# Kernel tuning notes

Hardware: AMD Instinct MI355X
Metric: run time of the kernel (lower is better)

The kernel has to match this reference:

```python
import jax, jax.numpy as jnp
import numpy as np

N_NODES = 30000
N_EDGES = 480000
N_REL = 16
DIM = 128
N_TRIPLES = 200000


def _xavier(key, shape):
    fan_in, fan_out = shape[-2], shape[-1]
    limit = np.sqrt(6.0 / (fan_in + fan_out)).astype(np.float32)
    return jax.random.uniform(key, shape, jnp.float32, -limit, limit)


def setup_inputs() -> dict:
    key = jax.random.key(0)
    ks = jax.random.split(key, 12)
    inp = {
        "node_emb": _xavier(ks[0], (N_NODES, DIM)),
        "rel_emb": _xavier(ks[1], (N_REL, DIM)),
        "W_rel0": _xavier(ks[2], (N_REL, DIM, DIM)),
        "Wself_w0": _xavier(ks[3], (DIM, DIM)),
        "Wself_b0": jnp.zeros((DIM,), jnp.float32),
        "W_rel1": _xavier(ks[4], (N_REL, DIM, DIM)),
        "Wself_w1": _xavier(ks[5], (DIM, DIM)),
        "Wself_b1": jnp.zeros((DIM,), jnp.float32),
        "local_nodes": jnp.arange(N_NODES, dtype=jnp.int32),
        "edge_index": jax.random.randint(ks[6], (2, N_EDGES), 0, N_NODES, jnp.int32),
        "edge_type": jax.random.randint(ks[7], (N_EDGES,), 0, N_REL, jnp.int32),
        "h_loc": jax.random.randint(ks[8], (N_TRIPLES,), 0, N_NODES, jnp.int32),
        "r_ids": jax.random.randint(ks[9], (N_TRIPLES,), 0, N_REL, jnp.int32),
        "t_loc": jax.random.randint(ks[10], (N_TRIPLES,), 0, N_NODES, jnp.int32),
    }
    return inp


def _rgcn_layer(x, edge_index, edge_type, W_rel, Ww, Wb):
    # x: [N, in], W_rel: [R, in, out], Ww: [out, in] (torch Linear layout)
    N = x.shape[0]
    out = x @ Ww.T + Wb                                 # self loop [N, out]
    src, dst = edge_index[0], edge_index[1]
    # transform every node under every relation, then gather per edge:
    # math-equivalent to bmm(x[src][:,None,:], W_rel[rel]) in the original,
    # but avoids materializing [E, in, out].
    xt = jnp.einsum('ni,rio->rno', x, W_rel)            # [R, N, out]
    msg = xt[edge_type, src]                            # [E, out]
    agg = jax.ops.segment_sum(msg, dst, num_segments=N)  # [N, out]
    deg = jax.ops.segment_sum(jnp.ones(dst.shape, x.dtype), dst, num_segments=N)
    deg = jnp.maximum(deg, 1.0)[:, None]
    return jax.nn.relu(out + agg / deg)


def reference(node_emb, rel_emb, W_rel0, Wself_w0, Wself_b0,
              W_rel1, Wself_w1, Wself_b1,
              local_nodes, edge_index, edge_type, h_loc, r_ids, t_loc):
    x = node_emb[local_nodes]                           # [N, d]
    x = _rgcn_layer(x, edge_index, edge_type, W_rel0, Wself_w0, Wself_b0)
    x = _rgcn_layer(x, edge_index, edge_type, W_rel1, Wself_w1, Wself_b1)
    # DistMult scoring on local embeddings
    scores = jnp.sum(x[h_loc] * rel_emb[r_ids] * x[t_loc], axis=-1)  # [B]
    return scores
```

## Files before the change

kernel.cpp:

```cpp
#include <hip/hip_runtime.h>

#define NN 30000
#define NE 480000
#define NR 16
#define D  128
#define NT 200000
#define BR 64
#define NBLK 469
#define NBINS (NBLK * NR)
#define PF 24


__global__ void k_gather_x(const float* __restrict__ node_emb,
                           const int* __restrict__ local_nodes,
                           float* __restrict__ x) {
  int i4 = blockIdx.x * blockDim.x + threadIdx.x;
  if (i4 >= NN * (D / 4)) return;
  int n = i4 >> 5, c = i4 & 31;
  int src = local_nodes[n];
  reinterpret_cast<float4*>(x)[i4] =
      reinterpret_cast<const float4*>(node_emb)[(size_t)src * 32 + c];
}

__global__ void k_hist_bins(const int* __restrict__ ei, const int* __restrict__ et,
                            int* __restrict__ bins) {
  int e = blockIdx.x * blockDim.x + threadIdx.x;
  if (e >= NE) return;
  int d = ei[NE + e], r = et[e];
  atomicAdd(&bins[(d >> 6) * NR + r], 1);
}

__global__ void k_scan_bins(const int* __restrict__ bins, int* __restrict__ off,
                            int* __restrict__ cur) {
  __shared__ int ps[1024];
  const int t = threadIdx.x;
  const int base = t * 8;
  int c[8], s0 = 0;
#pragma unroll
  for (int u = 0; u < 8; ++u) {
    int b = base + u;
    c[u] = (b < NBINS) ? bins[b] : 0;
    s0 += c[u];
  }
  ps[t] = s0;
  __syncthreads();
  for (int dstep = 1; dstep < 1024; dstep <<= 1) {
    int v = (t >= dstep) ? ps[t - dstep] : 0;
    __syncthreads();
    ps[t] += v;
    __syncthreads();
  }
  int ex = ps[t] - s0;
#pragma unroll
  for (int u = 0; u < 8; ++u) {
    int b = base + u;
    if (b <= NBINS) {
      off[b] = ex;
      if (b < NBINS) cur[b] = ex;
    }
    ex += c[u];
  }
}

__global__ void k_fill(const int* __restrict__ ei, const int* __restrict__ et,
                       int* __restrict__ cur, int* __restrict__ srt,
                       float* __restrict__ deg) {
  int e = blockIdx.x * blockDim.x + threadIdx.x;
  if (e >= NE) return;
  int s = ei[e], d = ei[NE + e], r = et[e];
  int p = atomicAdd(&cur[(d >> 6) * NR + r], 1);
  srt[p] = ((d & 63) << 16) | s;
  atomicAdd(&deg[d], 1.0f);
}

__global__ void k_transposeW(const float* __restrict__ W0, const float* __restrict__ W1,
                             float* __restrict__ T0, float* __restrict__ T1) {
  const float* W = blockIdx.x ? W1 : W0;
  float* T = blockIdx.x ? T1 : T0;
  for (int idx = threadIdx.x; idx < D * D; idx += 256) {
    int o = idx >> 7, k = idx & 127;
    T[k * D + o] = W[idx];
  }
}


__device__ __forceinline__ void gemm_tile(const float (*S)[D],
                                          const float* __restrict__ Wg,
                                          int tx, int ty, float acc[8][4]) {
  const float4* __restrict__ W4 = reinterpret_cast<const float4*>(Wg);
#pragma unroll 8
  for (int k = 0; k < D; k += 4) {
    float4 a[8];
#pragma unroll
    for (int j = 0; j < 8; ++j)
      a[j] = *reinterpret_cast<const float4*>(&S[ty + 8 * j][k]);
    float4 w[4];
#pragma unroll
    for (int kk = 0; kk < 4; ++kk) w[kk] = W4[(k + kk) * 32 + tx];
#pragma unroll
    for (int kk = 0; kk < 4; ++kk) {
#pragma unroll
      for (int j = 0; j < 8; ++j) {
        float av = (kk == 0) ? a[j].x : (kk == 1) ? a[j].y
                 : (kk == 2) ? a[j].z : a[j].w;
        acc[j][0] += av * w[kk].x;
        acc[j][1] += av * w[kk].y;
        acc[j][2] += av * w[kk].z;
        acc[j][3] += av * w[kk].w;
      }
    }
  }
}

__launch_bounds__(256, 2)
__global__ void k_fused(const float* __restrict__ x, const float* __restrict__ Wrel,
                        const float* __restrict__ WT, const float* __restrict__ Wb,
                        const int* __restrict__ srt, const int* __restrict__ off,
                        const float* __restrict__ deg, float* __restrict__ xo) {
  __shared__ float S[2][BR][D];
  const int nb = blockIdx.x;
  const int row0 = nb * BR;
  const int tx = threadIdx.x & 31, ty = threadIdx.x >> 5;
  const int wave = threadIdx.x >> 6, lane = threadIdx.x & 63;
  const float2* __restrict__ x2 = reinterpret_cast<const float2*>(x);

  float acc[8][4];
#pragma unroll
  for (int j = 0; j < 8; ++j)
#pragma unroll
    for (int m = 0; m < 4; ++m) acc[j][m] = 0.f;

  int pv[PF];
  float2 pvv[PF];

  auto zeroS = [&](int c) {
    float4* S4 = reinterpret_cast<float4*>(&S[c][0][0]);
#pragma unroll
    for (int t = 0; t < 8; ++t)
      S4[threadIdx.x + 256 * t] = make_float4(0.f, 0.f, 0.f, 0.f);
  };
  auto loadE = [&](int b) {
    const int base = off[b], end = off[b + 1];
#pragma unroll
    for (int t = 0; t < PF; ++t) {
      int i = base + wave + 4 * t;
      pv[t] = (i < end) ? srt[i] : -1;
    }
#pragma unroll
    for (int t = 0; t < PF; ++t)
      pvv[t] = (pv[t] >= 0) ? x2[(size_t)(pv[t] & 0xFFFF) * 64 + lane]
                            : make_float2(0.f, 0.f);
  };
  auto depositE = [&](int b, int c) {
#pragma unroll
    for (int t = 0; t < PF; ++t)
      if (pv[t] >= 0) {
        int dl = pv[t] >> 16;
        atomicAdd(&S[c][dl][2 * lane], pvv[t].x);
        atomicAdd(&S[c][dl][2 * lane + 1], pvv[t].y);
      }
    const int end = off[b + 1];
    for (int i = off[b] + 4 * PF + wave; i < end; i += 4) {
      int p = srt[i];
      float2 vv = x2[(size_t)(p & 0xFFFF) * 64 + lane];
      atomicAdd(&S[c][p >> 16][2 * lane], vv.x);
      atomicAdd(&S[c][p >> 16][2 * lane + 1], vv.y);
    }
  };

  zeroS(0);
  zeroS(1);
  __syncthreads();
  loadE(nb * NR);
  depositE(nb * NR, 0);

  int cur = 0;
  for (int r = 0; r < NR; ++r) {
    __syncthreads();
    if (r + 1 < NR) loadE(nb * NR + r + 1);
    gemm_tile(S[cur], Wrel + (size_t)r * D * D, tx, ty, acc);
    if (r + 1 < NR) depositE(nb * NR + r + 1, cur ^ 1);
    __syncthreads();
    if (r + 2 < NR) zeroS(cur);
    cur ^= 1;
  }

#pragma unroll
  for (int j = 0; j < 8; ++j) {
    int row = row0 + ty + 8 * j;
    float dv = (row < NN) ? deg[row] : 1.f;
    float inv = 1.f / fmaxf(dv, 1.f);
#pragma unroll
    for (int m = 0; m < 4; ++m) acc[j][m] *= inv;
  }

#pragma unroll
  for (int t = 0; t < 8; ++t) {
    int idx = threadIdx.x + 256 * t;
    int rw = idx >> 5, c = idx & 31;
    float4 vv = make_float4(0.f, 0.f, 0.f, 0.f);
    if (row0 + rw < NN)
      vv = reinterpret_cast<const float4*>(x)[(size_t)(row0 + rw) * 32 + c];
    *reinterpret_cast<float4*>(&S[0][rw][4 * c]) = vv;
  }
  __syncthreads();
  gemm_tile(S[0], WT, tx, ty, acc);

  const float4 bb = reinterpret_cast<const float4*>(Wb)[tx];
#pragma unroll
  for (int j = 0; j < 8; ++j) {
    int row = row0 + ty + 8 * j;
    if (row < NN) {
      float4 o;
      o.x = fmaxf(acc[j][0] + bb.x, 0.f);
      o.y = fmaxf(acc[j][1] + bb.y, 0.f);
      o.z = fmaxf(acc[j][2] + bb.z, 0.f);
      o.w = fmaxf(acc[j][3] + bb.w, 0.f);
      reinterpret_cast<float4*>(xo + (size_t)row * D)[tx] = o;
    }
  }
}


__global__ void k_score(const float* __restrict__ x, const float* __restrict__ rel,
                        const int* __restrict__ hh, const int* __restrict__ rr,
                        const int* __restrict__ tt, float* __restrict__ out) {
  int gw = (blockIdx.x * blockDim.x + threadIdx.x) >> 6;
  int lane = threadIdx.x & 63;
  int nw = (gridDim.x * blockDim.x) >> 6;
  for (int i = gw; i < NT; i += nw) {
    const float2* ph = reinterpret_cast<const float2*>(x + (size_t)hh[i] * D);
    const float2* pr = reinterpret_cast<const float2*>(rel + (size_t)rr[i] * D);
    const float2* pt = reinterpret_cast<const float2*>(x + (size_t)tt[i] * D);
    float2 a = ph[lane], b = pr[lane], c = pt[lane];
    float v = a.x * b.x * c.x + a.y * b.y * c.y;
#pragma unroll
    for (int m = 32; m; m >>= 1) v += __shfl_xor(v, m);
    if (lane == 0) out[i] = v;
  }
}


extern "C" void kernel_launch(void* const* d_in, const int* in_sizes, int n_in,
                              void* d_out, int out_size, void* d_ws, size_t ws_size,
                              hipStream_t stream) {
  const float* node_emb = (const float*)d_in[0];
  const float* rel_emb  = (const float*)d_in[1];
  const float* W_rel0   = (const float*)d_in[2];
  const float* Wself_w0 = (const float*)d_in[3];
  const float* Wself_b0 = (const float*)d_in[4];
  const float* W_rel1   = (const float*)d_in[5];
  const float* Wself_w1 = (const float*)d_in[6];
  const float* Wself_b1 = (const float*)d_in[7];
  const int* local_nodes = (const int*)d_in[8];
  const int* edge_index  = (const int*)d_in[9];
  const int* edge_type   = (const int*)d_in[10];
  const int* h_loc = (const int*)d_in[11];
  const int* r_ids = (const int*)d_in[12];
  const int* t_loc = (const int*)d_in[13];
  float* out = (float*)d_out;

  char* ws = (char*)d_ws;
  float* x_a = (float*)(ws + 0);
  float* x_b = (float*)(ws + 15360000);
  float* WT0 = (float*)(ws + 30720000);
  float* WT1 = (float*)(ws + 30785536);
  float* deg = (float*)(ws + 30851072);
  int* bins  = (int*)(ws + 30971072);
  int* off   = (int*)(ws + 31001088);
  int* cur   = (int*)(ws + 31031108);
  int* srt   = (int*)(ws + 31061124);
  if (ws_size < (size_t)32981124) return;

  hipMemsetAsync(ws + 30851072, 0, 150016, stream);

  k_gather_x<<<3750, 256, 0, stream>>>(node_emb, local_nodes, x_a);
  k_hist_bins<<<1875, 256, 0, stream>>>(edge_index, edge_type, bins);
  k_scan_bins<<<1, 1024, 0, stream>>>(bins, off, cur);
  k_fill<<<1875, 256, 0, stream>>>(edge_index, edge_type, cur, srt, deg);
  k_transposeW<<<2, 256, 0, stream>>>(Wself_w0, Wself_w1, WT0, WT1);

  k_fused<<<NBLK, 256, 0, stream>>>(x_a, W_rel0, WT0, Wself_b0, srt, off, deg, x_b);
  k_fused<<<NBLK, 256, 0, stream>>>(x_b, W_rel1, WT1, Wself_b1, srt, off, deg, x_a);

  k_score<<<1024, 256, 0, stream>>>(x_a, rel_emb, h_loc, r_ids, t_loc, out);
}
```

Baseline: 1.417 ms.

## Stage edge gathers via async global-to-LDS loads with a single accumulation buffer

Replaces the register-held prefetch of gathered neighbour rows with asynchronous global_load_lds copies into a shared staging buffer G, plus a small per-slot destination array. The next relation's gathers are issued before the current GEMM so the copies overlap the matrix work. The double-buffered accumulation tile becomes a single buffer that is deposited before the GEMM and zeroed after it. This frees many vector registers that held prefetched data, but adds LDS footprint, an extra barrier per relation, and makes the deposit step run serially with the GEMM.

```diff
diff --git a/kernel.cpp b/kernel.cpp
--- a/kernel.cpp
+++ b/kernel.cpp
@@ -8,7 +8,8 @@
 #define BR 64
 #define NBLK 469
 #define NBINS (NBLK * NR)
-#define PF 24
+#define GS 92
+#define PF 23
 
 
 __global__ void k_gather_x(const float* __restrict__ node_emb,
@@ -83,6 +84,12 @@
   }
 }
 
+__device__ __forceinline__ void gl_lds4(const float* g, float* l) {
+  __builtin_amdgcn_global_load_lds(
+      (const __attribute__((address_space(1))) void*)g,
+      (__attribute__((address_space(3))) void*)l, 4, 0, 0);
+}
+
 
 __device__ __forceinline__ void gemm_tile(const float (*S)[D],
                                           const float* __restrict__ Wg,
@@ -117,7 +124,9 @@
                         const float* __restrict__ WT, const float* __restrict__ Wb,
                         const int* __restrict__ srt, const int* __restrict__ off,
                         const float* __restrict__ deg, float* __restrict__ xo) {
-  __shared__ float S[2][BR][D];
+  __shared__ float S[BR][D];
+  __shared__ float G[GS][D];
+  __shared__ int dls[GS];
   const int nb = blockIdx.x;
   const int row0 = nb * BR;
   const int tx = threadIdx.x & 31, ty = threadIdx.x >> 5;
@@ -130,59 +139,62 @@
 #pragma unroll
     for (int m = 0; m < 4; ++m) acc[j][m] = 0.f;
 
-  int pv[PF];
-  float2 pvv[PF];
-
-  auto zeroS = [&](int c) {
-    float4* S4 = reinterpret_cast<float4*>(&S[c][0][0]);
+  auto zeroS = [&]() {
+    float4* S4 = reinterpret_cast<float4*>(&S[0][0]);
 #pragma unroll
     for (int t = 0; t < 8; ++t)
       S4[threadIdx.x + 256 * t] = make_float4(0.f, 0.f, 0.f, 0.f);
   };
-  auto loadE = [&](int b) {
+
+  auto issueDMA = [&](int b) {
     const int base = off[b], end = off[b + 1];
 #pragma unroll
     for (int t = 0; t < PF; ++t) {
-      int i = base + wave + 4 * t;
-      pv[t] = (i < end) ? srt[i] : -1;
-    }
-#pragma unroll
-    for (int t = 0; t < PF; ++t)
-      pvv[t] = (pv[t] >= 0) ? x2[(size_t)(pv[t] & 0xFFFF) * 64 + lane]
-                            : make_float2(0.f, 0.f);
+      int s = wave + 4 * t;
+      int i = base + s;
+      int p = (i < end) ? srt[i] : -1;
+      if (lane == 0) dls[s] = p;
+      if (p >= 0) {
+        const float* row = x + (size_t)(p & 0xFFFF) * D;
+        gl_lds4(row + lane, &G[s][0]);
+        gl_lds4(row + 64 + lane, &G[s][64]);
+      }
+    }
   };
-  auto depositE = [&](int b, int c) {
-#pragma unroll
-    for (int t = 0; t < PF; ++t)
-      if (pv[t] >= 0) {
-        int dl = pv[t] >> 16;
-        atomicAdd(&S[c][dl][2 * lane], pvv[t].x);
-        atomicAdd(&S[c][dl][2 * lane + 1], pvv[t].y);
+  auto depositE = [&](int b) {
+#pragma unroll
+    for (int t = 0; t < PF; ++t) {
+      int s = wave + 4 * t;
+      int p = dls[s];
+      if (p >= 0) {
+        float2 v = *reinterpret_cast<const float2*>(&G[s][2 * lane]);
+        atomicAdd(&S[p >> 16][2 * lane], v.x);
+        atomicAdd(&S[p >> 16][2 * lane + 1], v.y);
       }
+    }
     const int end = off[b + 1];
-    for (int i = off[b] + 4 * PF + wave; i < end; i += 4) {
+    for (int i = off[b] + GS + wave; i < end; i += 4) {
       int p = srt[i];
       float2 vv = x2[(size_t)(p & 0xFFFF) * 64 + lane];
-      atomicAdd(&S[c][p >> 16][2 * lane], vv.x);
-      atomicAdd(&S[c][p >> 16][2 * lane + 1], vv.y);
+      atomicAdd(&S[p >> 16][2 * lane], vv.x);
+      atomicAdd(&S[p >> 16][2 * lane + 1], vv.y);
     }
   };
 
-  zeroS(0);
-  zeroS(1);
+  zeroS();
+  issueDMA(nb * NR);
   __syncthreads();
-  loadE(nb * NR);
-  depositE(nb * NR, 0);
-
-  int cur = 0;
+
   for (int r = 0; r < NR; ++r) {
-    __syncthreads();
-    if (r + 1 < NR) loadE(nb * NR + r + 1);
-    gemm_tile(S[cur], Wrel + (size_t)r * D * D, tx, ty, acc);
-    if (r + 1 < NR) depositE(nb * NR + r + 1, cur ^ 1);
-    __syncthreads();
-    if (r + 2 < NR) zeroS(cur);
-    cur ^= 1;
+    depositE(nb * NR + r);
+    __syncthreads();
+    if (r + 1 < NR) issueDMA(nb * NR + r + 1);
+    gemm_tile(S, Wrel + (size_t)r * D * D, tx, ty, acc);
+    __syncthreads();
+    if (r + 1 < NR) {
+      zeroS();
+      __syncthreads();
+    }
   }
 
 #pragma unroll
@@ -201,10 +213,10 @@
     float4 vv = make_float4(0.f, 0.f, 0.f, 0.f);
     if (row0 + rw < NN)
       vv = reinterpret_cast<const float4*>(x)[(size_t)(row0 + rw) * 32 + c];
-    *reinterpret_cast<float4*>(&S[0][rw][4 * c]) = vv;
+    *reinterpret_cast<float4*>(&S[rw][4 * c]) = vv;
   }
   __syncthreads();
-  gemm_tile(S[0], WT, tx, ty, acc);
+  gemm_tile(S, WT, tx, ty, acc);
 
   const float4 bb = reinterpret_cast<const float4*>(Wb)[tx];
 #pragma unroll
```

New measurement: 1.449 ms. 2.3% more time.
